# Optimization experiments

Hardware: AMD Instinct MI355X
Metric: run time of the kernel (lower is better)

## Reference

```python
import jax, jax.numpy as jnp
import numpy as np

X, Y = 128, 128           # SOM grid rows/cols
F = 512                   # num_features
B = 2048                  # batch_size
SIGMA = 1.0               # gaussian neighborhood width
LR = 0.5                  # learning rate


def setup_inputs() -> dict:
    key = jax.random.key(0)
    k1, k2 = jax.random.split(key)
    data = jax.random.normal(k1, (B, F), dtype=jnp.float32)
    # init like the module: 2*randn - 1, then L2-normalize along features
    w = 2.0 * jax.random.normal(k2, (X, Y, F), dtype=jnp.float32) - 1.0
    weights = w / jnp.linalg.norm(w, axis=-1, keepdims=True)
    return {"data": data, "weights": weights}


def reference(data, weights):
    # --- distances to all neurons (squared euclidean; argmin is sqrt-invariant) ---
    w_flat = weights.reshape(X * Y, F)                       # [XY, F]
    d2 = ((data * data).sum(-1, keepdims=True)               # [B, 1]
          + (w_flat * w_flat).sum(-1)[None, :]               # [1, XY]
          - 2.0 * jnp.einsum("bf,nf->bn", data, w_flat))    # [B, XY]
    idx = jnp.argmin(d2, axis=1)                             # [B]
    bmu_row = idx // Y
    bmu_col = idx % Y

    # --- gaussian neighborhood around each BMU on the rectangular meshgrid ---
    rows = jnp.arange(X, dtype=jnp.float32)                  # xx axis
    cols = jnp.arange(Y, dtype=jnp.float32)                  # yy axis
    dr2 = (rows[None, :] - bmu_row[:, None].astype(jnp.float32)) ** 2   # [B, X]
    dc2 = (cols[None, :] - bmu_col[:, None].astype(jnp.float32)) ** 2   # [B, Y]
    denom = 2.0 * SIGMA * SIGMA
    neigh = jnp.exp(-(dr2[:, :, None] + dc2[:, None, :]) / denom)       # [B, X, Y]

    # --- mean weighted update, without materializing [B, X, Y, F] ---
    # mean_b lr*n_b*(d_b - W) = lr*(mean_b n_b*d_b - (mean_b n_b)*W)
    nd_mean = jnp.einsum("bxy,bf->xyf", neigh, data) / B     # [X, Y, F]
    n_mean = neigh.mean(axis=0)                              # [X, Y]
    new_weights = weights + LR * (nd_mean - n_mean[:, :, None] * weights)
    return new_weights
```

## Files before the change

kernel.cpp:

```cpp
#include <hip/hip_runtime.h>


typedef __attribute__((ext_vector_type(8))) short          bf16x8;
typedef __attribute__((ext_vector_type(4))) float          f32x4;
typedef __attribute__((ext_vector_type(8))) unsigned short u16x8;

#define MFMA(a, b, c) __builtin_amdgcn_mfma_f32_16x16x32_bf16((a), (b), (c), 0, 0, 0)

static constexpr int GX = 128, GY = 128, NF = 512, NB = 2048, NXY = GX * GY;
static constexpr int RWIN = 5;
static constexpr float LR = 0.5f;

__device__ inline unsigned short f2bf(float x) {
    unsigned u = __float_as_uint(x);
    unsigned r = u + 0x7FFFu + ((u >> 16) & 1u);
    return (unsigned short)(r >> 16);
}
__device__ inline unsigned fkey(float f) {
    unsigned u = __float_as_uint(f);
    return (u & 0x80000000u) ? ~u : (u | 0x80000000u);
}
__device__ inline void glds16(const void* g, void* l) {
    __builtin_amdgcn_global_load_lds(
        (const __attribute__((address_space(1))) unsigned int*)g,
        (__attribute__((address_space(3))) unsigned int*)l, 16, 0, 0);
}

__global__ __launch_bounds__(256) void k_split(
    const float* __restrict__ A, unsigned short* __restrict__ Abf,
    const float* __restrict__ W, unsigned short* __restrict__ Wbf,
    unsigned long long* __restrict__ bmukey) {
    if (blockIdx.x == 4608) {
        int t = threadIdx.x;
#pragma unroll
        for (int j = 0; j < 8; ++j) bmukey[t * 8 + j] = ~0ull;
        return;
    }
    if (blockIdx.x < 512) {
        int i = blockIdx.x * 256 + threadIdx.x;
        const float4* a4 = (const float4*)A;
        float4 v0 = a4[2 * i], v1 = a4[2 * i + 1];
        float f[8] = {v0.x, v0.y, v0.z, v0.w, v1.x, v1.y, v1.z, v1.w};
        u16x8 h;
#pragma unroll
        for (int j = 0; j < 8; ++j) h[j] = (short)f2bf(f[j]);
        *(u16x8*)(Abf + (size_t)i * 8) = h;
    } else {
        int row  = (blockIdx.x - 512) * 4 + (threadIdx.x >> 6);
        int lane = threadIdx.x & 63;
        const float4* r4 = (const float4*)(W + (size_t)row * NF);
        float4 v0 = r4[lane * 2], v1 = r4[lane * 2 + 1];
        float f[8] = {v0.x, v0.y, v0.z, v0.w, v1.x, v1.y, v1.z, v1.w};
        u16x8 h;
#pragma unroll
        for (int j = 0; j < 8; ++j) h[j] = (short)f2bf(f[j]);
        *(u16x8*)(Wbf + (size_t)row * NF + lane * 8) = h;
    }
}

__global__ __launch_bounds__(512, 2) void k_gemm(
    const unsigned short* __restrict__ Abf, const unsigned short* __restrict__ Wbf,
    unsigned long long* __restrict__ bmukey) {
    __shared__ unsigned short lds[2][2][256 * 32];

    const int tid = threadIdx.x, lane = tid & 63, w = tid >> 6;
    const int wr = w >> 1, wc = w & 1;
    const int b = blockIdx.x;
    const int xcd = b & 7, idx = b >> 3;
    const int n0 = (((xcd << 3) | (idx & 7))) * 256;
    const int m0 = (idx >> 3) * 256;

    const int cc0 = tid, cc1 = 512 + tid;
    const int r0 = cc0 >> 2, u0 = (cc0 & 3) ^ ((r0 >> 1) & 3);
    const int r1 = cc1 >> 2, u1 = (cc1 & 3) ^ ((r1 >> 1) & 3);
    const int offA0 = (m0 + r0) * NF + u0 * 8, offA1 = (m0 + r1) * NF + u1 * 8;
    const int offB0 = (n0 + r0) * NF + u0 * 8, offB1 = (n0 + r1) * NF + u1 * 8;
    unsigned short* lbase0 = &lds[0][0][0];
    unsigned short* lbase1 = &lds[1][0][0];

#define STAGE(B, T)                                                            \
    do {                                                                       \
        const int kt_ = (T) * 32;                                              \
        unsigned short* ld_ = (B) ? lbase1 : lbase0;                           \
        glds16(Abf + offA0 + kt_, ld_ + cc0 * 8);                              \
        glds16(Abf + offA1 + kt_, ld_ + cc1 * 8);                              \
        glds16(Wbf + offB0 + kt_, ld_ + 8192 + cc0 * 8);                       \
        glds16(Wbf + offB1 + kt_, ld_ + 8192 + cc1 * 8);                       \
    } while (0)

    int aoff[4], boff[8];
#pragma unroll
    for (int m = 0; m < 4; ++m) {
        int row = wr * 64 + m * 16 + (lane & 15);
        int s   = (lane >> 4) ^ ((row >> 1) & 3);
        aoff[m] = row * 32 + s * 8;
    }
#pragma unroll
    for (int n = 0; n < 8; ++n) {
        int row = wc * 128 + n * 16 + (lane & 15);
        int s   = (lane >> 4) ^ ((row >> 1) & 3);
        boff[n] = 8192 + row * 32 + s * 8;
    }

    f32x4 acc[4][8];
#pragma unroll
    for (int m = 0; m < 4; ++m)
#pragma unroll
        for (int n = 0; n < 8; ++n) acc[m][n] = (f32x4){0.f, 0.f, 0.f, 0.f};

#define COMPUTE(B)                                                             \
    do {                                                                       \
        unsigned short* lb_ = (B) ? lbase1 : lbase0;                           \
        bf16x8 af[4], bf[4];                                                   \
        _Pragma("unroll") for (int m = 0; m < 4; ++m)                          \
            af[m] = *(const bf16x8*)(lb_ + aoff[m]);                           \
        _Pragma("unroll") for (int n = 0; n < 4; ++n)                          \
            bf[n] = *(const bf16x8*)(lb_ + boff[n]);                           \
        __builtin_amdgcn_s_setprio(1);                                         \
        _Pragma("unroll") for (int n = 0; n < 4; ++n)                          \
            _Pragma("unroll") for (int m = 0; m < 4; ++m)                      \
                acc[m][n] = MFMA(af[m], bf[n], acc[m][n]);                     \
        __builtin_amdgcn_s_setprio(0);                                         \
        _Pragma("unroll") for (int n = 0; n < 4; ++n)                          \
            bf[n] = *(const bf16x8*)(lb_ + boff[n + 4]);                       \
        __builtin_amdgcn_s_setprio(1);                                         \
        _Pragma("unroll") for (int n = 0; n < 4; ++n)                          \
            _Pragma("unroll") for (int m = 0; m < 4; ++m)                      \
                acc[m][n + 4] = MFMA(af[m], bf[n], acc[m][n + 4]);             \
        __builtin_amdgcn_s_setprio(0);                                         \
    } while (0)

    STAGE(0, 0);
    __syncthreads();
#pragma unroll 1
    for (int t = 0; t < 16; t += 2) {
        if (t + 1 < 16) STAGE(1, t + 1);
        COMPUTE(0);
        __syncthreads();
        if (t + 2 < 16) STAGE(0, t + 2);
        COMPUTE(1);
        __syncthreads();
    }

#pragma unroll
    for (int m = 0; m < 4; ++m)
#pragma unroll
        for (int reg = 0; reg < 4; ++reg) {
            int grow = m0 + wr * 64 + m * 16 + (lane >> 4) * 4 + reg;
            unsigned long long key = ~0ull;
#pragma unroll
            for (int n = 0; n < 8; ++n) {
                unsigned long long k2 =
                    ((unsigned long long)fkey(-acc[m][n][reg]) << 32) |
                    (unsigned)(n0 + wc * 128 + n * 16 + (lane & 15));
                key = (k2 < key) ? k2 : key;
            }
#pragma unroll
            for (int mask = 1; mask <= 8; mask <<= 1) {
                unsigned long long o = __shfl_xor(key, mask);
                key = (o < key) ? o : key;
            }
            if ((lane & 15) == 0) atomicMin(bmukey + grow, key);
        }
#undef STAGE
#undef COMPUTE
}

__global__ __launch_bounds__(1024) void k_bin(
    const unsigned long long* __restrict__ bmukey,
    int* __restrict__ counts, int* __restrict__ offsets,
    int* __restrict__ cinfo, int* __restrict__ occ_cell,
    int* __restrict__ n_occ, int* __restrict__ list) {
    __shared__ int sbmu[NB];
    __shared__ int scnt[NXY];
    __shared__ int soff[NXY];
    __shared__ int ws[16], wo[16];
    const int t = threadIdx.x, lane = t & 63, w = t >> 6;

    for (int i = t; i < NXY; i += 1024) scnt[i] = 0;
    for (int i = t; i < NB; i += 1024) sbmu[i] = (int)(bmukey[i] & 0xFFFFFFFFull);
    __syncthreads();
    for (int i = t; i < NB; i += 1024) atomicAdd(&scnt[sbmu[i]], 1);
    __syncthreads();

    const int base = t * 16;
    int sc = 0, so = 0;
#pragma unroll
    for (int i = 0; i < 16; ++i) { int c = scnt[base + i]; sc += c; so += (c != 0); }
    int vs = sc, vo = so;
#pragma unroll
    for (int d = 1; d < 64; d <<= 1) {
        int us = __shfl_up(vs, d), uo = __shfl_up(vo, d);
        if (lane >= d) { vs += us; vo += uo; }
    }
    if (lane == 63) { ws[w] = vs; wo[w] = vo; }
    __syncthreads();
    if (t == 0) {
        int rs = 0, ro = 0;
        for (int i = 0; i < 16; ++i) {
            int a = ws[i]; ws[i] = rs; rs += a;
            int c = wo[i]; wo[i] = ro; ro += c;
        }
        n_occ[0] = ro;
    }
    __syncthreads();
    int es = vs - sc + ws[w];
    int eo = vo - so + wo[w];
    for (int i = 0; i < 16; ++i) {
        int cell = base + i, c = scnt[cell];
        soff[cell] = es;
        offsets[cell] = es;
        cinfo[cell] = (c << 16) | eo;
        counts[cell] = c;
        if (c) { occ_cell[eo] = cell; eo++; }
        es += c;
    }
    __syncthreads();

    if (w == 0) {
        for (int g = 0; g < 32; ++g) {
            int bb = g * 64 + lane;
            int key = sbmu[bb];
            unsigned long long match = ~0ull;
#pragma unroll
            for (int j = 0; j < 14; ++j) {
                unsigned long long bj = __ballot((key >> j) & 1);
                match &= ((key >> j) & 1) ? bj : ~bj;
            }
            unsigned long long below = ((unsigned long long)1 << lane) - 1;
            int rin = __popcll(match & below);
            int bse = soff[key];
            if (rin == 0) soff[key] = bse + __popcll(match);
            list[bse + rin] = bb;
        }
    }
}

__global__ __launch_bounds__(256) void k_gc(const float* __restrict__ data,
                                            const int* __restrict__ counts,
                                            const int* __restrict__ offsets,
                                            const int* __restrict__ list,
                                            const int* __restrict__ occ_cell,
                                            const int* __restrict__ n_occ,
                                            float* __restrict__ Gc) {
    int s = blockIdx.x;
    if (s >= n_occ[0]) return;
    int cell = occ_cell[s];
    int cnt = counts[cell], off = offsets[cell];
    int t = threadIdx.x;
    float ax = 0.f, ay = 0.f;
    for (int i = 0; i < cnt; ++i) {
        int b = list[off + i];
        float2 d = ((const float2*)data)[b * 256 + t];
        ax += d.x;
        ay += d.y;
    }
    float2 g = {ax, ay};
    ((float2*)Gc)[(size_t)s * 256 + t] = g;
}

__global__ __launch_bounds__(256) void k_update(
    const float* __restrict__ W, const float* __restrict__ Gc,
    const int* __restrict__ cinfo, float* __restrict__ out) {
    __shared__ float swgt[128], scw[128];
    __shared__ int sslot[128];
    __shared__ int scnt0, scnt1;
    const int n = blockIdx.x;
    const int x = n >> 7, y = n & 127;
    const int t = threadIdx.x, w = t >> 6, lane = t & 63;

    bool valid = false;
    float wgt = 0.f;
    int slot = 0, cnt = 0, rin = 0;
    if (t < 128) {
        if (t < 121) {
            int dx = t / 11 - RWIN, dy = t % 11 - RWIN;
            int bx = x + dx, by = y + dy;
            if ((unsigned)bx < 128u && (unsigned)by < 128u) {
                int info = cinfo[(bx << 7) | by];
                if (info > 0xFFFF) {
                    valid = true;
                    cnt = info >> 16;
                    slot = info & 0xFFFF;
                    wgt = __expf(-0.5f * (float)(dx * dx + dy * dy));
                }
            }
        }
        unsigned long long m = __ballot(valid);
        rin = __popcll(m & (((unsigned long long)1 << lane) - 1ull));
        if (lane == 0) { if (w == 0) scnt0 = __popcll(m); else scnt1 = __popcll(m); }
    }
    __syncthreads();
    if (valid) {
        int pos = rin + (w ? scnt0 : 0);
        sslot[pos] = slot;
        swgt[pos] = wgt;
        scw[pos] = wgt * (float)cnt;
    }
    __syncthreads();
    const int nocc = scnt0 + scnt1;

    float nd0 = 0.f, nd1 = 0.f, nwt = 0.f;
    const float2* gc2 = (const float2*)Gc;
    for (int e = 0; e < nocc; ++e) {
        float wg = swgt[e];
        int s = sslot[e];
        float2 g = gc2[s * 256 + t];
        nd0 += wg * g.x;
        nd1 += wg * g.y;
        nwt += scw[e];
    }

    float2 w2 = ((const float2*)W)[(size_t)n * 256 + t];
    const float c = LR / (float)NB;
    float2 o;
    o.x = w2.x + c * (nd0 - nwt * w2.x);
    o.y = w2.y + c * (nd1 - nwt * w2.y);
    ((float2*)out)[(size_t)n * 256 + t] = o;
}

extern "C" void kernel_launch(void* const* d_in, const int* in_sizes, int n_in,
                              void* d_out, int out_size, void* d_ws, size_t ws_size,
                              hipStream_t stream) {
    const float* data = (const float*)d_in[0];
    const float* W    = (const float*)d_in[1];
    float* out = (float*)d_out;
    char* ws = (char*)d_ws;

    unsigned short* Abf = (unsigned short*)(ws + 0);
    float*          Gc  = (float*)(ws + 0);
    unsigned long long* bmukey = (unsigned long long*)(ws + 4259840);
    int* counts   = (int*)(ws + 4276224);
    int* offsets  = (int*)(ws + 4341760);
    int* cinfo    = (int*)(ws + 4407296);
    int* occ_cell = (int*)(ws + 4472832);
    int* list     = (int*)(ws + 4481024);
    int* n_occ    = (int*)(ws + 4489216);

    unsigned short* Wbf = (unsigned short*)d_out;

    k_split<<<4609, 256, 0, stream>>>(data, Abf, W, Wbf, bmukey);

    k_gemm<<<512, 512, 0, stream>>>(Abf, Wbf, bmukey);

    k_bin<<<1, 1024, 0, stream>>>(bmukey, counts, offsets, cinfo, occ_cell,
                                  n_occ, list);
    k_gc<<<NB, 256, 0, stream>>>(data, counts, offsets, list, occ_cell, n_occ, Gc);
    k_update<<<NXY, 256, 0, stream>>>(W, Gc, cinfo, out);
}
```

Measured before the change: 151.4 us.

## Process eight adjacent neurons per block in update kernel to reuse Gc loads

The update kernel now handles a strip of 8 consecutive grid cells per block instead of one. It gathers occupied BMU cells over an 11x18 window, builds per-output separable Gaussian weights in shared memory, and accumulates 8 outputs per thread. Each Gc row load is then reused across 8 neurons, cutting redundant global reads from the overlapping 11x11 windows. In exchange each block does more setup work and holds more registers for the accumulators.

```diff
diff --git a/kernel.cpp b/kernel.cpp
--- a/kernel.cpp
+++ b/kernel.cpp
@@ -262,61 +262,92 @@
 __global__ __launch_bounds__(256) void k_update(
     const float* __restrict__ W, const float* __restrict__ Gc,
     const int* __restrict__ cinfo, float* __restrict__ out) {
-    __shared__ float swgt[128], scw[128];
-    __shared__ int sslot[128];
-    __shared__ int scnt0, scnt1;
-    const int n = blockIdx.x;
-    const int x = n >> 7, y = n & 127;
+    __shared__ int sslot[200];
+    __shared__ float srow[200], srowcnt[200];
+    __shared__ int sbyd[200];
+    __shared__ float swf[1600], swfc[1600];
+    __shared__ float nwt8[8];
+    __shared__ int wcnt[4];
+    const int x = blockIdx.x >> 4, y0 = (blockIdx.x & 15) << 3;
     const int t = threadIdx.x, w = t >> 6, lane = t & 63;
 
     bool valid = false;
-    float wgt = 0.f;
-    int slot = 0, cnt = 0, rin = 0;
-    if (t < 128) {
-        if (t < 121) {
-            int dx = t / 11 - RWIN, dy = t % 11 - RWIN;
-            int bx = x + dx, by = y + dy;
-            if ((unsigned)bx < 128u && (unsigned)by < 128u) {
-                int info = cinfo[(bx << 7) | by];
-                if (info > 0xFFFF) {
-                    valid = true;
-                    cnt = info >> 16;
-                    slot = info & 0xFFFF;
-                    wgt = __expf(-0.5f * (float)(dx * dx + dy * dy));
-                }
+    float rowfac = 0.f;
+    int slot = 0, cnt = 0, byd = 0;
+    if (t < 198) {
+        int bx = x - RWIN + t / 18;
+        int by = y0 - RWIN + t % 18;
+        if ((unsigned)bx < 128u && (unsigned)by < 128u) {
+            int info = cinfo[(bx << 7) | by];
+            if (info > 0xFFFF) {
+                valid = true;
+                cnt = info >> 16;
+                slot = info & 0xFFFF;
+                int dx = x - bx;
+                rowfac = __expf(-0.5f * (float)(dx * dx));
+                byd = by - y0;
             }
         }
-        unsigned long long m = __ballot(valid);
-        rin = __popcll(m & (((unsigned long long)1 << lane) - 1ull));
-        if (lane == 0) { if (w == 0) scnt0 = __popcll(m); else scnt1 = __popcll(m); }
-    }
-    __syncthreads();
+    }
+    unsigned long long m = __ballot(valid);
+    int rin = __popcll(m & (((unsigned long long)1 << lane) - 1ull));
+    if (lane == 0) wcnt[w] = __popcll(m);
+    __syncthreads();
+    int pre = 0;
+    for (int i = 0; i < w; ++i) pre += wcnt[i];
     if (valid) {
-        int pos = rin + (w ? scnt0 : 0);
+        int pos = pre + rin;
         sslot[pos] = slot;
-        swgt[pos] = wgt;
-        scw[pos] = wgt * (float)cnt;
-    }
-    __syncthreads();
-    const int nocc = scnt0 + scnt1;
-
-    float nd0 = 0.f, nd1 = 0.f, nwt = 0.f;
+        srow[pos] = rowfac;
+        srowcnt[pos] = rowfac * (float)cnt;
+        sbyd[pos] = byd;
+    }
+    __syncthreads();
+    const int ne = wcnt[0] + wcnt[1] + wcnt[2] + wcnt[3];
+
+    for (int idx = t; idx < ne * 8; idx += 256) {
+        int e = idx >> 3, o = idx & 7;
+        int d = sbyd[e] - o;
+        float cf = ((unsigned)(d + RWIN) <= 2u * RWIN)
+                       ? __expf(-0.5f * (float)(d * d)) : 0.f;
+        swf[idx] = srow[e] * cf;
+        swfc[idx] = srowcnt[e] * cf;
+    }
+    __syncthreads();
+    if (t < 8) {
+        float s = 0.f;
+        for (int e = 0; e < ne; ++e) s += swfc[e * 8 + t];
+        nwt8[t] = s;
+    }
+    __syncthreads();
+
+    float2 acc[8];
+#pragma unroll
+    for (int o = 0; o < 8; ++o) acc[o] = (float2){0.f, 0.f};
     const float2* gc2 = (const float2*)Gc;
-    for (int e = 0; e < nocc; ++e) {
-        float wg = swgt[e];
-        int s = sslot[e];
-        float2 g = gc2[s * 256 + t];
-        nd0 += wg * g.x;
-        nd1 += wg * g.y;
-        nwt += scw[e];
-    }
-
-    float2 w2 = ((const float2*)W)[(size_t)n * 256 + t];
+    for (int e = 0; e < ne; ++e) {
+        float2 g = gc2[sslot[e] * 256 + t];
+#pragma unroll
+        for (int o = 0; o < 8; ++o) {
+            float f = swf[e * 8 + o];
+            acc[o].x += f * g.x;
+            acc[o].y += f * g.y;
+        }
+    }
+
     const float c = LR / (float)NB;
-    float2 o;
-    o.x = w2.x + c * (nd0 - nwt * w2.x);
-    o.y = w2.y + c * (nd1 - nwt * w2.y);
-    ((float2*)out)[(size_t)n * 256 + t] = o;
+    const float2* W2 = (const float2*)W;
+    float2* O2 = (float2*)out;
+#pragma unroll
+    for (int o = 0; o < 8; ++o) {
+        size_t n = (size_t)((x << 7) | (y0 + o));
+        float2 w2 = W2[n * 256 + t];
+        float nw = nwt8[o];
+        float2 r;
+        r.x = w2.x + c * (acc[o].x - nw * w2.x);
+        r.y = w2.y + c * (acc[o].y - nw * w2.y);
+        O2[n * 256 + t] = r;
+    }
 }
 
 extern "C" void kernel_launch(void* const* d_in, const int* in_sizes, int n_in,
@@ -346,5 +377,5 @@
     k_bin<<<1, 1024, 0, stream>>>(bmukey, counts, offsets, cinfo, occ_cell,
                                   n_occ, list);
     k_gc<<<NB, 256, 0, stream>>>(data, counts, offsets, list, occ_cell, n_occ, Gc);
-    k_update<<<NXY, 256, 0, stream>>>(W, Gc, cinfo, out);
-}
+    k_update<<<2048, 256, 0, stream>>>(W, Gc, cinfo, out);
+}
```

Result: faster. 130.9 us, median of 2 (-13.6%).
